# Kernel optimization log

Hardware: AMD Instinct MI355X
Metric: run time of the kernel (lower is better)

Reference implementation:

```python
import jax, jax.numpy as jnp
import numpy as np

INPUT_DIM = 4096
BOTTLENECK = 32768
A = 2
K = 0.05
# eval-mode sparsity count: max(1, int(bottleneck * a * k))
K_COUNT = max(1, int(BOTTLENECK * A * K))  # 3276


def setup_inputs() -> dict:
    key = jax.random.key(0)
    kx, kw = jax.random.split(key)
    x = jax.random.normal(kx, (4096, INPUT_DIM), dtype=jnp.float32)
    # encoder weight [bottleneck, input_dim], like nn.Linear(input_dim, bottleneck)
    W = jax.random.normal(kw, (BOTTLENECK, INPUT_DIM), dtype=jnp.float32) * (1.0 / np.sqrt(INPUT_DIM))
    b_enc = jnp.zeros((BOTTLENECK,), dtype=jnp.float32)
    b_dec = jnp.zeros((INPUT_DIM,), dtype=jnp.float32)
    return {"x": x, "W": W, "b_enc": b_enc, "b_dec": b_dec, "epoch": 0}


def reference(x, W, b_enc, b_dec, epoch):
    # encode: z1 = x @ W^T + b_enc  -> [B, bottleneck]
    z1 = jnp.einsum("bi,hi->bh", x, W) + b_enc
    # eval-mode k-winner-take-all mask over dim 1
    _, topk_idx = jax.lax.top_k(z1, K_COUNT)  # [B, K_COUNT]
    rows = jnp.arange(z1.shape[0])[:, None]
    mask = jnp.zeros_like(z1).at[rows, topk_idx].set(1.0)
    a1 = z1 * mask
    # tied-weight decode: z2 = a1 @ W + b_dec -> [B, input_dim]
    z2 = jnp.einsum("bh,hi->bi", a1, W) + b_dec
    return z2
```

## Files before the change

kernel.cpp:

```cpp
#include <hip/hip_runtime.h>
#include <hip/hip_bf16.h>
#include <stdint.h>


#define DIM      4096
#define BATCH    4096
#define NROWS_W  32768
#define KCNT     3276
#define DELTA    0.0025f
#define ROWCAP   256
#define HCAP     64
#define CANDCAP  3584

typedef _Float16 f16x8 __attribute__((ext_vector_type(8)));
typedef _Float16 f16x4 __attribute__((ext_vector_type(4)));
typedef float    f32x4 __attribute__((ext_vector_type(4)));

__device__ __forceinline__ void gload_lds16(const void* g, void* l) {
  __builtin_amdgcn_global_load_lds(
      (const __attribute__((address_space(1))) void*)g,
      (__attribute__((address_space(3))) void*)l, 16, 0, 0);
}

__global__ void k_cvtx(const float* __restrict__ s, _Float16* __restrict__ hi, int n4) {
  int i = blockIdx.x * 256 + threadIdx.x;
  const int stride = gridDim.x * 256;
  for (; i < n4; i += stride) {
    f32x4 v = ((const f32x4*)s)[i];
    f16x4 h;
#pragma unroll
    for (int j = 0; j < 4; ++j) h[j] = (_Float16)v[j];
    ((f16x4*)hi)[i] = h;
  }
}

__global__ void k_splitw(const float* __restrict__ W, _Float16* __restrict__ Wh,
                         _Float16* __restrict__ Wt, f32x4* __restrict__ bcntv) {
  __shared__ _Float16 t[64][65];
  const int c0 = blockIdx.x * 64, r0 = blockIdx.y * 64;
  const int tx = threadIdx.x, ty = threadIdx.y;
  if (blockIdx.y == 0) {
    const int idx = blockIdx.x * 512 + ty * 64 + tx;
    if (idx < 8192) {
      f32x4 z = {0.f, 0.f, 0.f, 0.f};
      bcntv[idx] = z;
    }
  }
  for (int rr = ty; rr < 64; rr += 8) {
    const float w = W[(long)(r0 + rr) * DIM + c0 + tx];
    const _Float16 h = (_Float16)w;
    Wh[(long)(r0 + rr) * DIM + c0 + tx] = h;
    t[rr][tx] = h;
  }
  __syncthreads();
  for (int cc = ty; cc < 64; cc += 8)
    Wt[(long)(c0 + cc) * NROWS_W + r0 + tx] = t[tx][cc];
}

template <int MT, int NTOT, int KT, int SML, int SNL>
__global__ __launch_bounds__(256, 2)
void k_gemm(const _Float16* __restrict__ A, const _Float16* __restrict__ B,
            const float* __restrict__ bias, float* __restrict__ C) {
  constexpr int BM = 128, BN = 128, BK = 64;
  __shared__ __align__(16) _Float16 sA[BM * BK];
  __shared__ __align__(16) _Float16 sB[BN * BK];

  const int tid = threadIdx.x;
  constexpr int nbm = MT / BM, nbn = NTOT / BN;
  constexpr int grid = nbm * nbn;
  constexpr int nstn = nbn >> SNL;
  constexpr int stsz = 1 << (SML + SNL);

  int wg = blockIdx.x;
  wg = (wg & 7) * (grid >> 3) + (wg >> 3);
  const int g = wg >> (SML + SNL), r = wg & (stsz - 1);
  const int bm = ((g / nstn) << SML) + (r >> SNL);
  const int bn = ((g % nstn) << SNL) + (r & ((1 << SNL) - 1));

  const int m0 = bm * BM, n0 = bn * BN;
  const int lane = tid & 63, wid = tid >> 6;
  const int wm = wid >> 1, wn = wid & 1;
  const int lr = lane & 15, lk = lane >> 4;
  const int swz = (lr & 7) << 4;

  f32x4 acc[4][4] = {};

  for (int k0 = 0; k0 < KT; k0 += BK) {
#pragma unroll
    for (int rr = 0; rr < 4; ++rr) {
      const int o = (rr * 256 + tid) * 16;
      const int row = o >> 7;
      const int colb = (o & 127) ^ ((row & 7) << 4);
      const long gA = ((long)(m0 + row) * KT + k0) * 2 + colb;
      const long gB = ((long)(n0 + row) * KT + k0) * 2 + colb;
      gload_lds16((const char*)A + gA, (char*)sA + o);
      gload_lds16((const char*)B + gB, (char*)sB + o);
    }
    __syncthreads();

#pragma unroll
    for (int kk = 0; kk < 2; ++kk) {
      f16x8 va[4], vb[4];
      const int kbase = (kk * 64 + lk * 16) ^ swz;
#pragma unroll
      for (int m = 0; m < 4; ++m) {
        const int row = wm * 64 + m * 16 + lr;
        va[m] = *(const f16x8*)((const char*)sA + row * 128 + kbase);
      }
#pragma unroll
      for (int n = 0; n < 4; ++n) {
        const int row = wn * 64 + n * 16 + lr;
        vb[n] = *(const f16x8*)((const char*)sB + row * 128 + kbase);
      }
#pragma unroll
      for (int m = 0; m < 4; ++m)
#pragma unroll
        for (int n = 0; n < 4; ++n)
          acc[m][n] = __builtin_amdgcn_mfma_f32_16x16x32_f16(va[m], vb[n], acc[m][n], 0, 0, 0);
    }
    __syncthreads();
  }

#pragma unroll
  for (int n = 0; n < 4; ++n) {
    const int col = n0 + wn * 64 + n * 16 + lr;
    const float bv = bias[col];
#pragma unroll
    for (int m = 0; m < 4; ++m) {
      const int r0r = m0 + wm * 64 + m * 16 + lk * 4;
#pragma unroll
      for (int j = 0; j < 4; ++j)
        C[(long)(r0r + j) * NTOT + col] = acc[m][n][j] + bv;
    }
  }
}

__device__ __forceinline__ unsigned f2o(float f) {
  unsigned b = __float_as_uint(f);
  return ((int)b < 0) ? ~b : (b | 0x80000000u);
}
__device__ __forceinline__ float o2f(unsigned u) {
  unsigned b = (u & 0x80000000u) ? (u & 0x7FFFFFFFu) : ~u;
  return __uint_as_float(b);
}

__global__ __launch_bounds__(256)
void k_topk4(const float* __restrict__ z1, float* __restrict__ thr,
             unsigned* __restrict__ rowlist, unsigned* __restrict__ rowcnt,
             unsigned* __restrict__ c1, unsigned* __restrict__ bucket,
             unsigned* __restrict__ bcnt, _Float16* __restrict__ a1,
             float* __restrict__ candv, unsigned short* __restrict__ candi,
             unsigned* __restrict__ candn, int kwant) {
  __shared__ unsigned hist[4096];
  __shared__ float cv[CANDCAP];
  __shared__ unsigned short ci[CANDCAP];
  __shared__ unsigned s_n, s_bin, s_rem, s_wt[4], s_cnt, s_above;
  const int tid = threadIdx.x;
  const int b = blockIdx.x;
  const f32x4* zv = (const f32x4*)(z1 + (long)b * NROWS_W);
  constexpr int NV = NROWS_W / 4;

#pragma unroll
  for (int j = 0; j < 16; ++j) hist[tid + j * 256] = 0;
  if (tid == 0) { s_n = 0; s_cnt = 0; s_above = 0; }
  __syncthreads();
  for (int i = tid; i < NV; i += 256) {
    f32x4 v = zv[i];
#pragma unroll
    for (int j = 0; j < 4; ++j) atomicAdd(&hist[f2o(v[j]) >> 20], 1u);
  }
  __syncthreads();
  unsigned p = 0;
#pragma unroll
  for (int j = 0; j < 16; ++j) p += hist[tid * 16 + j];
  unsigned sfx = p;
  const int lane = tid & 63, w = tid >> 6;
#pragma unroll
  for (int off = 1; off < 64; off <<= 1) {
    unsigned o = __shfl_down(sfx, off);
    sfx += (lane + off < 64) ? o : 0u;
  }
  if (lane == 0) s_wt[w] = sfx;
  __syncthreads();
  unsigned above_waves = 0;
  for (int ww = w + 1; ww < 4; ++ww) above_waves += s_wt[ww];
  const unsigned incl = sfx + above_waves;
  const int cnt = __syncthreads_count(incl >= (unsigned)kwant);
  const int tstar = cnt - 1;
  if (tid == tstar) {
    unsigned cum = incl - p;
    int bsel = tid * 16;
    for (int j = 15; j >= 0; --j) {
      const unsigned h = hist[tid * 16 + j];
      if (cum + h >= (unsigned)kwant) { bsel = tid * 16 + j; break; }
      cum += h;
    }
    s_bin = (unsigned)bsel;
    s_rem = (unsigned)kwant - cum;
  }
  __syncthreads();
  const unsigned binsel = s_bin;
  unsigned rem = s_rem;

  {
    unsigned loc = 0;
#pragma unroll
    for (int j = 0; j < 16; ++j) {
      const unsigned bin = tid * 16 + j;
      if (bin >= binsel + 2) loc += hist[bin];
    }
    if (loc) atomicAdd(&s_above, loc);
  }

  const unsigned blo = (binsel > 0) ? binsel - 1 : 0;
  const unsigned bhi = (binsel < 4095) ? binsel + 1 : 4095;
  f16x4* av = (f16x4*)(a1 + (long)b * NROWS_W);
  for (int i = tid; i < NV; i += 256) {
    f32x4 v = zv[i];
    f16x4 o;
#pragma unroll
    for (int j = 0; j < 4; ++j) {
      const unsigned bin = f2o(v[j]) >> 20;
      o[j] = (bin > bhi) ? (_Float16)v[j] : (_Float16)0.0f;
      if (bin >= blo && bin <= bhi) {
        const unsigned jj = atomicAdd(&s_n, 1u);
        if (jj < CANDCAP) { cv[jj] = v[j]; ci[jj] = (unsigned short)(i * 4 + j); }
      }
    }
    av[i] = o;
  }
  __syncthreads();
  const int n = (s_n < CANDCAP) ? (int)s_n : CANDCAP;
  if (tid == 0) candn[b] = (unsigned)n;
  for (int i = tid; i < n; i += 256) {
    candv[(long)b * CANDCAP + i] = cv[i];
    candi[(long)b * CANDCAP + i] = ci[i];
  }

  unsigned pfx = 0;
#pragma unroll
  for (int pass = 0; pass < 3; ++pass) {
    const int shift = (pass == 0) ? 12 : (pass == 1) ? 4 : 0;
    const int nb = (pass == 2) ? 16 : 256;
    if (tid < 256) hist[tid] = 0;
    __syncthreads();
    for (int i = tid; i < n; i += 256) {
      const unsigned u = f2o(cv[i]);
      if ((u >> 20) != binsel) continue;
      const unsigned v = u & 0xFFFFFu;
      const bool m = (pass == 0) ? true
                     : (pass == 1) ? ((v >> 12) == (pfx >> 12))
                                   : ((v >> 4) == (pfx >> 4));
      if (m) atomicAdd(&hist[(v >> shift) & (nb - 1)], 1u);
    }
    __syncthreads();
    if (tid == 0) {
      unsigned cum = 0;
      int d = nb - 1;
      for (; d > 0; --d) {
        if (cum + hist[d] >= rem) break;
        cum += hist[d];
      }
      s_bin = (unsigned)d;
      s_rem = rem - cum;
    }
    __syncthreads();
    pfx |= (s_bin << shift);
    rem = s_rem;
    __syncthreads();
  }
  const float t = o2f((binsel << 20) | pfx);
  if (tid == 0) thr[b] = t;
  const float hi = t + DELTA, lo = t - DELTA;

  for (int i = tid; i < n; i += 256) {
    const float v = cv[i];
    if (v >= lo && v <= hi) {
      const unsigned idx = ci[i];
      const unsigned jj = atomicAdd(&s_cnt, 1u);
      if (jj < ROWCAP) {
        rowlist[(long)b * ROWCAP + jj] = idx;
        const unsigned pq = atomicAdd(&bcnt[idx], 1u);
        if (pq < HCAP) bucket[(long)idx * HCAP + pq] = ((unsigned)b << 9) | jj;
      }
    }
  }
  __syncthreads();
  if (tid == 0) {
    rowcnt[b] = (s_cnt < ROWCAP) ? s_cnt : ROWCAP;
    c1[b] = s_above;
  }
}

__global__ void k_recompute(const float* __restrict__ W, const float* __restrict__ x,
                            const unsigned* __restrict__ bucket,
                            const unsigned* __restrict__ bcnt,
                            float* __restrict__ exact) {
  const int h = blockIdx.x;
  unsigned n = bcnt[h];
  if (n > HCAP) n = HCAP;
  if (n == 0) return;
  __shared__ float wrec[DIM];
  const long wb = (long)h * DIM;
  for (int i = threadIdx.x; i < DIM / 4; i += 256)
    ((f32x4*)wrec)[i] = ((const f32x4*)(W + wb))[i];
  __syncthreads();
  const int w = threadIdx.x >> 6, lane = threadIdx.x & 63;
  for (unsigned e = w; e < n; e += 4) {
    const unsigned ent = bucket[(long)h * HCAP + e];
    const int b = ent >> 9, j = ent & 511;
    const f32x4* xv = (const f32x4*)(x + (long)b * DIM);
    float s = 0.f;
#pragma unroll
    for (int c = 0; c < 16; ++c) {
      const int i4 = c * 64 + lane;
      f32x4 v = xv[i4];
      const float* wr = &wrec[i4 * 4];
#pragma unroll
      for (int q = 0; q < 4; ++q) s += v[q] * wr[q];
    }
#pragma unroll
    for (int m = 32; m; m >>= 1) s += __shfl_xor(s, m);
    if (lane == 0) exact[(long)b * ROWCAP + j] = s;
  }
}

__global__ void k_select(const float* __restrict__ exact, const unsigned* __restrict__ rowlist,
                         const unsigned* __restrict__ rowcnt, const unsigned* __restrict__ c1,
                         const float* __restrict__ thr, const float* __restrict__ candv,
                         const unsigned short* __restrict__ candi,
                         const unsigned* __restrict__ candn,
                         const float* __restrict__ z1, _Float16* __restrict__ a1) {
  const int b = blockIdx.x;
  const int n = (int)rowcnt[b];
  const int nc = (int)candn[b];
  const float t = thr[b];
  const float hi = t + DELTA;
  __shared__ float vals[ROWCAP];
  __shared__ unsigned s_c;
  const int j = threadIdx.x;
  if (j == 0) s_c = 0;
  vals[j] = (j < n) ? exact[(long)b * ROWCAP + j] : -1e30f;
  __syncthreads();
  unsigned loc = 0;
  for (int i = j; i < nc; i += 256) loc += (candv[(long)b * CANDCAP + i] > hi) ? 1u : 0u;
  if (loc) atomicAdd(&s_c, loc);
  __syncthreads();
  const int need = KCNT - (int)c1[b] - (int)s_c;
  if (j < n) {
    const float vj = vals[j];
    int rank = 0;
    for (int i = 0; i < n; ++i) {
      const float vi = vals[i];
      rank += (vi > vj || (vi == vj && i < j)) ? 1 : 0;
    }
    if (rank < need) {
      const unsigned h = rowlist[(long)b * ROWCAP + j];
      const long off = (long)b * NROWS_W + h;
      a1[off] = (_Float16)z1[off];
    }
  }
  for (int i = j; i < nc; i += 256) {
    const float v = candv[(long)b * CANDCAP + i];
    if (v > hi) a1[(long)b * NROWS_W + candi[(long)b * CANDCAP + i]] = (_Float16)v;
  }
}

extern "C" void kernel_launch(void* const* d_in, const int* in_sizes, int n_in,
                              void* d_out, int out_size, void* d_ws, size_t ws_size,
                              hipStream_t stream) {
  const float* x     = (const float*)d_in[0];
  const float* W     = (const float*)d_in[1];
  const float* b_enc = (const float*)d_in[2];
  const float* b_dec = (const float*)d_in[3];
  float* out = (float*)d_out;

  const long NW = (long)NROWS_W * DIM;
  const long NX = (long)BATCH * DIM;
  const long NZ = (long)BATCH * NROWS_W;

  char* ws = (char*)d_ws;
  _Float16* Wh = (_Float16*)ws;
  _Float16* Wt = Wh + NW;
  _Float16* xh = Wt + NW;
  float*  z1 = (float*)(xh + NX);
  float*  thr = z1 + NZ;
  char*   sc = (char*)(thr + BATCH);
  unsigned* rowcnt  = (unsigned*)sc;
  unsigned* c1      = (unsigned*)(sc + 16384);
  unsigned* bcnt    = (unsigned*)(sc + 32768);
  float*    exact   = (float*)(sc + 163840);
  unsigned* rowlist = (unsigned*)(sc + 4358144);
  unsigned* bucket  = (unsigned*)(sc + 8552448);
  unsigned* candn   = (unsigned*)(sc + 16941056);
  float*    candv   = (float*)(sc + 16957440);
  unsigned short* candi = (unsigned short*)(sc + 75677696);
  _Float16* a1 = Wh;

  const size_t needed = (size_t)(4 * NW + 2 * NX) + (size_t)4 * NZ + 4 * BATCH + 106000000;
  if (ws_size < needed) return;

  k_splitw<<<dim3(DIM / 64, NROWS_W / 64), dim3(64, 8), 0, stream>>>(W, Wh, Wt, (f32x4*)bcnt);
  k_cvtx<<<2048, 256, 0, stream>>>(x, xh, (int)(NX / 4));

  k_gemm<BATCH, NROWS_W, DIM, 4, 5>
      <<<(BATCH / 128) * (NROWS_W / 128), 256, 0, stream>>>(xh, Wh, b_enc, z1);

  k_topk4<<<BATCH, 256, 0, stream>>>(z1, thr, rowlist, rowcnt, c1, bucket, bcnt,
                                     a1, candv, candi, candn, KCNT);
  k_recompute<<<NROWS_W, 256, 0, stream>>>(W, x, bucket, bcnt, exact);
  k_select<<<BATCH, ROWCAP, 0, stream>>>(exact, rowlist, rowcnt, c1, thr,
                                         candv, candi, candn, z1, a1);

  k_gemm<BATCH, DIM, NROWS_W, 4, 3>
      <<<(BATCH / 128) * (DIM / 128), 256, 0, stream>>>(a1, Wt, b_dec, out);
}
```

Before: 3.433 ms.

## Store encoder output as fp16 and run top-k selection on fp16 keys

The first GEMM now writes z1 as fp16 instead of fp32. The top-k kernel reads 8 halves per vector load and histograms directly on 16-bit order keys, which collapses the multi-pass radix refinement into a single 16-bin pass. The candidate buffer shrinks, the band delta widens, boundary values come from the exact recompute (bias now added there) instead of rereading z1, and the XCD block remapping is dropped with the decode GEMM swizzle changed. This halves z1 memory traffic and simplifies selection, but fp16 quantization of z1 coarsens the threshold and relies on the recompute band to resolve ties, with overflow risk if more than 512 candidates land near the threshold.

```diff
diff --git a/kernel.cpp b/kernel.cpp
--- a/kernel.cpp
+++ b/kernel.cpp
@@ -1,5 +1,6 @@
 #include <hip/hip_runtime.h>
 #include <hip/hip_bf16.h>
+#include <hip/hip_fp16.h>
 #include <stdint.h>
 
 
@@ -7,14 +8,15 @@
 #define BATCH    4096
 #define NROWS_W  32768
 #define KCNT     3276
-#define DELTA    0.0025f
+#define DELTA    0.005f
 #define ROWCAP   256
 #define HCAP     64
-#define CANDCAP  3584
+#define CANDCAP  512
 
 typedef _Float16 f16x8 __attribute__((ext_vector_type(8)));
 typedef _Float16 f16x4 __attribute__((ext_vector_type(4)));
 typedef float    f32x4 __attribute__((ext_vector_type(4)));
+typedef unsigned short u16x8 __attribute__((ext_vector_type(8)));
 
 __device__ __forceinline__ void gload_lds16(const void* g, void* l) {
   __builtin_amdgcn_global_load_lds(
@@ -57,23 +59,20 @@
     Wt[(long)(c0 + cc) * NROWS_W + r0 + tx] = t[tx][cc];
 }
 
-template <int MT, int NTOT, int KT, int SML, int SNL>
+template <int MT, int NTOT, int KT, int SML, int SNL, typename OutT>
 __global__ __launch_bounds__(256, 2)
 void k_gemm(const _Float16* __restrict__ A, const _Float16* __restrict__ B,
-            const float* __restrict__ bias, float* __restrict__ C) {
+            const float* __restrict__ bias, OutT* __restrict__ C) {
   constexpr int BM = 128, BN = 128, BK = 64;
   __shared__ __align__(16) _Float16 sA[BM * BK];
   __shared__ __align__(16) _Float16 sB[BN * BK];
 
   const int tid = threadIdx.x;
-  constexpr int nbm = MT / BM, nbn = NTOT / BN;
-  constexpr int grid = nbm * nbn;
+  constexpr int nbn = NTOT / BN;
   constexpr int nstn = nbn >> SNL;
   constexpr int stsz = 1 << (SML + SNL);
 
-  int wg = blockIdx.x;
-  wg = (wg & 7) * (grid >> 3) + (wg >> 3);
-  const int g = wg >> (SML + SNL), r = wg & (stsz - 1);
+  const int g = blockIdx.x >> (SML + SNL), r = blockIdx.x & (stsz - 1);
   const int bm = ((g / nstn) << SML) + (r >> SNL);
   const int bn = ((g % nstn) << SNL) + (r & ((1 << SNL) - 1));
 
@@ -130,44 +129,44 @@
       const int r0r = m0 + wm * 64 + m * 16 + lk * 4;
 #pragma unroll
       for (int j = 0; j < 4; ++j)
-        C[(long)(r0r + j) * NTOT + col] = acc[m][n][j] + bv;
-    }
-  }
-}
-
-__device__ __forceinline__ unsigned f2o(float f) {
-  unsigned b = __float_as_uint(f);
-  return ((int)b < 0) ? ~b : (b | 0x80000000u);
-}
-__device__ __forceinline__ float o2f(unsigned u) {
-  unsigned b = (u & 0x80000000u) ? (u & 0x7FFFFFFFu) : ~u;
-  return __uint_as_float(b);
+        C[(long)(r0r + j) * NTOT + col] = (OutT)(acc[m][n][j] + bv);
+    }
+  }
+}
+
+__device__ __forceinline__ unsigned f2o16(unsigned b) {
+  return (b & 0x8000u) ? (~b & 0xFFFFu) : (b | 0x8000u);
+}
+__device__ __forceinline__ float o2f16v(unsigned key) {
+  const unsigned short bb = (key & 0x8000u) ? (unsigned short)(key & 0x7FFFu)
+                                            : (unsigned short)(~key & 0xFFFFu);
+  return (float)__builtin_bit_cast(_Float16, bb);
 }
 
 __global__ __launch_bounds__(256)
-void k_topk4(const float* __restrict__ z1, float* __restrict__ thr,
-             unsigned* __restrict__ rowlist, unsigned* __restrict__ rowcnt,
-             unsigned* __restrict__ c1, unsigned* __restrict__ bucket,
-             unsigned* __restrict__ bcnt, _Float16* __restrict__ a1,
-             float* __restrict__ candv, unsigned short* __restrict__ candi,
-             unsigned* __restrict__ candn, int kwant) {
+void k_topk16(const unsigned short* __restrict__ z1b, float* __restrict__ thr,
+              unsigned* __restrict__ rowlist, unsigned* __restrict__ rowcnt,
+              unsigned* __restrict__ c1, unsigned* __restrict__ bucket,
+              unsigned* __restrict__ bcnt, unsigned short* __restrict__ a1b,
+              float* __restrict__ candv, unsigned short* __restrict__ candi,
+              unsigned* __restrict__ candn, int kwant) {
   __shared__ unsigned hist[4096];
   __shared__ float cv[CANDCAP];
   __shared__ unsigned short ci[CANDCAP];
   __shared__ unsigned s_n, s_bin, s_rem, s_wt[4], s_cnt, s_above;
   const int tid = threadIdx.x;
   const int b = blockIdx.x;
-  const f32x4* zv = (const f32x4*)(z1 + (long)b * NROWS_W);
-  constexpr int NV = NROWS_W / 4;
+  const u16x8* zv = (const u16x8*)(z1b + (long)b * NROWS_W);
+  constexpr int NV = NROWS_W / 8;
 
 #pragma unroll
   for (int j = 0; j < 16; ++j) hist[tid + j * 256] = 0;
   if (tid == 0) { s_n = 0; s_cnt = 0; s_above = 0; }
   __syncthreads();
   for (int i = tid; i < NV; i += 256) {
-    f32x4 v = zv[i];
-#pragma unroll
-    for (int j = 0; j < 4; ++j) atomicAdd(&hist[f2o(v[j]) >> 20], 1u);
+    u16x8 v = zv[i];
+#pragma unroll
+    for (int j = 0; j < 8; ++j) atomicAdd(&hist[f2o16(v[j]) >> 4], 1u);
   }
   __syncthreads();
   unsigned p = 0;
@@ -200,7 +199,7 @@
   }
   __syncthreads();
   const unsigned binsel = s_bin;
-  unsigned rem = s_rem;
+  const unsigned rem = s_rem;
 
   {
     unsigned loc = 0;
@@ -213,18 +212,22 @@
   }
 
   const unsigned blo = (binsel > 0) ? binsel - 1 : 0;
-  const unsigned bhi = (binsel < 4095) ? binsel + 1 : 4095;
-  f16x4* av = (f16x4*)(a1 + (long)b * NROWS_W);
+  const unsigned bhi = binsel + 1;
+  u16x8* av = (u16x8*)(a1b + (long)b * NROWS_W);
   for (int i = tid; i < NV; i += 256) {
-    f32x4 v = zv[i];
-    f16x4 o;
-#pragma unroll
-    for (int j = 0; j < 4; ++j) {
-      const unsigned bin = f2o(v[j]) >> 20;
-      o[j] = (bin > bhi) ? (_Float16)v[j] : (_Float16)0.0f;
+    u16x8 v = zv[i];
+    u16x8 o;
+#pragma unroll
+    for (int j = 0; j < 8; ++j) {
+      const unsigned bits = v[j];
+      const unsigned bin = f2o16(bits) >> 4;
+      o[j] = (bin > bhi) ? (unsigned short)bits : (unsigned short)0;
       if (bin >= blo && bin <= bhi) {
         const unsigned jj = atomicAdd(&s_n, 1u);
-        if (jj < CANDCAP) { cv[jj] = v[j]; ci[jj] = (unsigned short)(i * 4 + j); }
+        if (jj < CANDCAP) {
+          cv[jj] = (float)__builtin_bit_cast(_Float16, (unsigned short)bits);
+          ci[jj] = (unsigned short)(i * 8 + j);
+        }
       }
     }
     av[i] = o;
@@ -232,44 +235,29 @@
   __syncthreads();
   const int n = (s_n < CANDCAP) ? (int)s_n : CANDCAP;
   if (tid == 0) candn[b] = (unsigned)n;
+  if (tid < 16) hist[tid] = 0;
+  __syncthreads();
+
   for (int i = tid; i < n; i += 256) {
-    candv[(long)b * CANDCAP + i] = cv[i];
+    const float v = cv[i];
+    candv[(long)b * CANDCAP + i] = v;
     candi[(long)b * CANDCAP + i] = ci[i];
-  }
-
-  unsigned pfx = 0;
-#pragma unroll
-  for (int pass = 0; pass < 3; ++pass) {
-    const int shift = (pass == 0) ? 12 : (pass == 1) ? 4 : 0;
-    const int nb = (pass == 2) ? 16 : 256;
-    if (tid < 256) hist[tid] = 0;
-    __syncthreads();
-    for (int i = tid; i < n; i += 256) {
-      const unsigned u = f2o(cv[i]);
-      if ((u >> 20) != binsel) continue;
-      const unsigned v = u & 0xFFFFFu;
-      const bool m = (pass == 0) ? true
-                     : (pass == 1) ? ((v >> 12) == (pfx >> 12))
-                                   : ((v >> 4) == (pfx >> 4));
-      if (m) atomicAdd(&hist[(v >> shift) & (nb - 1)], 1u);
-    }
-    __syncthreads();
-    if (tid == 0) {
-      unsigned cum = 0;
-      int d = nb - 1;
-      for (; d > 0; --d) {
-        if (cum + hist[d] >= rem) break;
-        cum += hist[d];
-      }
-      s_bin = (unsigned)d;
-      s_rem = rem - cum;
-    }
-    __syncthreads();
-    pfx |= (s_bin << shift);
-    rem = s_rem;
-    __syncthreads();
-  }
-  const float t = o2f((binsel << 20) | pfx);
+    const unsigned short bb = __builtin_bit_cast(unsigned short, (_Float16)v);
+    const unsigned key = f2o16(bb);
+    if ((key >> 4) == binsel) atomicAdd(&hist[key & 15u], 1u);
+  }
+  __syncthreads();
+  if (tid == 0) {
+    unsigned cum = 0;
+    int d = 15;
+    for (; d > 0; --d) {
+      if (cum + hist[d] >= rem) break;
+      cum += hist[d];
+    }
+    s_bin = (unsigned)d;
+  }
+  __syncthreads();
+  const float t = o2f16v((binsel << 4) | s_bin);
   if (tid == 0) thr[b] = t;
   const float hi = t + DELTA, lo = t - DELTA;
 
@@ -293,6 +281,7 @@
 }
 
 __global__ void k_recompute(const float* __restrict__ W, const float* __restrict__ x,
+                            const float* __restrict__ b_enc,
                             const unsigned* __restrict__ bucket,
                             const unsigned* __restrict__ bcnt,
                             float* __restrict__ exact) {
@@ -305,6 +294,7 @@
   for (int i = threadIdx.x; i < DIM / 4; i += 256)
     ((f32x4*)wrec)[i] = ((const f32x4*)(W + wb))[i];
   __syncthreads();
+  const float be = b_enc[h];
   const int w = threadIdx.x >> 6, lane = threadIdx.x & 63;
   for (unsigned e = w; e < n; e += 4) {
     const unsigned ent = bucket[(long)h * HCAP + e];
@@ -321,7 +311,7 @@
     }
 #pragma unroll
     for (int m = 32; m; m >>= 1) s += __shfl_xor(s, m);
-    if (lane == 0) exact[(long)b * ROWCAP + j] = s;
+    if (lane == 0) exact[(long)b * ROWCAP + j] = s + be;
   }
 }
 
@@ -330,7 +320,7 @@
                          const float* __restrict__ thr, const float* __restrict__ candv,
                          const unsigned short* __restrict__ candi,
                          const unsigned* __restrict__ candn,
-                         const float* __restrict__ z1, _Float16* __restrict__ a1) {
+                         _Float16* __restrict__ a1) {
   const int b = blockIdx.x;
   const int n = (int)rowcnt[b];
   const int nc = (int)candn[b];
@@ -354,11 +344,8 @@
       const float vi = vals[i];
       rank += (vi > vj || (vi == vj && i < j)) ? 1 : 0;
     }
-    if (rank < need) {
-      const unsigned h = rowlist[(long)b * ROWCAP + j];
-      const long off = (long)b * NROWS_W + h;
-      a1[off] = (_Float16)z1[off];
-    }
+    if (rank < need)
+      a1[(long)b * NROWS_W + rowlist[(long)b * ROWCAP + j]] = (_Float16)vals[j];
   }
   for (int i = j; i < nc; i += 256) {
     const float v = candv[(long)b * CANDCAP + i];
@@ -383,8 +370,8 @@
   _Float16* Wh = (_Float16*)ws;
   _Float16* Wt = Wh + NW;
   _Float16* xh = Wt + NW;
-  float*  z1 = (float*)(xh + NX);
-  float*  thr = z1 + NZ;
+  _Float16* z1f = xh + NX;
+  float*  thr = (float*)(z1f + NZ);
   char*   sc = (char*)(thr + BATCH);
   unsigned* rowcnt  = (unsigned*)sc;
   unsigned* c1      = (unsigned*)(sc + 16384);
@@ -394,24 +381,25 @@
   unsigned* bucket  = (unsigned*)(sc + 8552448);
   unsigned* candn   = (unsigned*)(sc + 16941056);
   float*    candv   = (float*)(sc + 16957440);
-  unsigned short* candi = (unsigned short*)(sc + 75677696);
+  unsigned short* candi = (unsigned short*)(sc + 25346048);
   _Float16* a1 = Wh;
 
-  const size_t needed = (size_t)(4 * NW + 2 * NX) + (size_t)4 * NZ + 4 * BATCH + 106000000;
+  const size_t needed = (size_t)(4 * NW + 2 * NX + 2 * NZ) + 4 * BATCH + 29540352;
   if (ws_size < needed) return;
 
   k_splitw<<<dim3(DIM / 64, NROWS_W / 64), dim3(64, 8), 0, stream>>>(W, Wh, Wt, (f32x4*)bcnt);
   k_cvtx<<<2048, 256, 0, stream>>>(x, xh, (int)(NX / 4));
 
-  k_gemm<BATCH, NROWS_W, DIM, 4, 5>
-      <<<(BATCH / 128) * (NROWS_W / 128), 256, 0, stream>>>(xh, Wh, b_enc, z1);
-
-  k_topk4<<<BATCH, 256, 0, stream>>>(z1, thr, rowlist, rowcnt, c1, bucket, bcnt,
-                                     a1, candv, candi, candn, KCNT);
-  k_recompute<<<NROWS_W, 256, 0, stream>>>(W, x, bucket, bcnt, exact);
+  k_gemm<BATCH, NROWS_W, DIM, 4, 5, _Float16>
+      <<<(BATCH / 128) * (NROWS_W / 128), 256, 0, stream>>>(xh, Wh, b_enc, z1f);
+
+  k_topk16<<<BATCH, 256, 0, stream>>>((const unsigned short*)z1f, thr, rowlist,
+                                      rowcnt, c1, bucket, bcnt,
+                                      (unsigned short*)a1, candv, candi, candn, KCNT);
+  k_recompute<<<NROWS_W, 256, 0, stream>>>(W, x, b_enc, bucket, bcnt, exact);
   k_select<<<BATCH, ROWCAP, 0, stream>>>(exact, rowlist, rowcnt, c1, thr,
-                                         candv, candi, candn, z1, a1);
-
-  k_gemm<BATCH, DIM, NROWS_W, 4, 3>
+                                         candv, candi, candn, a1);
+
+  k_gemm<BATCH, DIM, NROWS_W, 4, 5, float>
       <<<(BATCH / 128) * (DIM / 128), 256, 0, stream>>>(a1, Wt, b_dec, out);
 }
```

Result: faster. 3.159 ms (-8.0%).
